# Optimization experiments

Measured on AMD Instinct MI355X. Metric: run time of the kernel, lower is better.

Reference implementation:

```python
import jax, jax.numpy as jnp
import numpy as np

C = 768; NUM_HEADS = 12; HID = 3072
HP = 14; WP = 14; TF = 8; BATCH = 4
EPS = 1e-5


def layer_norm(x, g, b):
    mu = jnp.mean(x, axis=-1, keepdims=True)
    var = jnp.mean((x - mu) ** 2, axis=-1, keepdims=True)
    return (x - mu) / jnp.sqrt(var + EPS) * g + b


def mha(x, qkv_w, qkv_b, proj_w, proj_b):
    # Manual multi-head softmax attention, faithful to Attention.forward.
    B, N, Cd = x.shape
    D = Cd // NUM_HEADS
    qkv = (x @ qkv_w.T + qkv_b).reshape(B, N, 3, NUM_HEADS, D).transpose(2, 0, 3, 1, 4)
    q, k, v = qkv[0], qkv[1], qkv[2]  # [B, H, N, D]
    attn = jax.nn.softmax(jnp.einsum('bhnd,bhmd->bhnm', q, k) * (D ** -0.5), axis=-1)
    out = jnp.einsum('bhnm,bhmd->bhnd', attn, v).transpose(0, 2, 1, 3).reshape(B, N, Cd)
    return out @ proj_w.T + proj_b


def setup_inputs() -> dict:
    key = jax.random.key(0)
    ks = jax.random.split(key, 16)
    p = lambda i, s: jax.random.normal(ks[i], s, jnp.float32) * 0.02
    N = 1 + HP * WP * TF  # cls token + spatial*temporal tokens
    return {
        'x': jax.random.normal(ks[0], (BATCH, N, C), jnp.float32),
        'ln_t_g': jnp.ones((C,), jnp.float32), 'ln_t_b': jnp.zeros((C,), jnp.float32),
        't_qkv_w': p(1, (3 * C, C)), 't_qkv_b': p(2, (3 * C,)),
        't_proj_w': p(3, (C, C)), 't_proj_b': p(4, (C,)),
        't_fc_w': p(5, (C, C)), 't_fc_b': p(6, (C,)),
        'ln1_g': jnp.ones((C,), jnp.float32), 'ln1_b': jnp.zeros((C,), jnp.float32),
        's_qkv_w': p(7, (3 * C, C)), 's_qkv_b': p(8, (3 * C,)),
        's_proj_w': p(9, (C, C)), 's_proj_b': p(10, (C,)),
        'ln2_g': jnp.ones((C,), jnp.float32), 'ln2_b': jnp.zeros((C,), jnp.float32),
        'fc1_w': p(11, (HID, C)), 'fc1_b': p(12, (HID,)),
        'fc2_w': p(13, (C, HID)), 'fc2_b': p(14, (C,)),
        'B': BATCH, 'T': TF, 'W': WP,
    }


def reference(x, ln_t_g, ln_t_b, t_qkv_w, t_qkv_b, t_proj_w, t_proj_b, t_fc_w, t_fc_b,
              ln1_g, ln1_b, s_qkv_w, s_qkv_b, s_proj_w, s_proj_b,
              ln2_g, ln2_b, fc1_w, fc1_b, fc2_w, fc2_b, B, T, W):
    # Block.forward, attention_type='divided_space_time', extra_tokens=0, is_cls=True.
    Bv, Ntot, Cd = x.shape
    H = ((Ntot - 1) // T) // W
    # --- temporal attention: 'b (h w t) m -> (b h w) t m' ---
    xt = x[:, 1:, :].reshape(B, H, W, T, Cd).reshape(B * H * W, T, Cd)
    res_t = mha(layer_norm(xt, ln_t_g, ln_t_b), t_qkv_w, t_qkv_b, t_proj_w, t_proj_b)
    res_t = res_t.reshape(B, H * W * T, Cd) @ t_fc_w.T + t_fc_b
    xt = x[:, 1:, :] + res_t  # [B, H*W*T, C]
    # --- spatial attention: 'b (h w t) m -> (b t) (h w) m' with cls token per frame ---
    init_cls = x[:, :1, :]  # [B, 1, C]
    cls_tok = jnp.repeat(init_cls, T, axis=1).reshape(B * T, 1, Cd)
    xs = xt.reshape(B, H, W, T, Cd).transpose(0, 3, 1, 2, 4).reshape(B * T, H * W, Cd)
    xs = jnp.concatenate([cls_tok, xs], axis=1)  # [(B*T), 1+H*W, C]
    res_s = mha(layer_norm(xs, ln1_g, ln1_b), s_qkv_w, s_qkv_b, s_proj_w, s_proj_b)
    cls_out = jnp.mean(res_s[:, 0, :].reshape(B, T, Cd), axis=1, keepdims=True)  # mean over frames
    res_s = res_s[:, 1:, :].reshape(B, T, H, W, Cd).transpose(0, 2, 3, 1, 4).reshape(B, H * W * T, Cd)
    x = jnp.concatenate([init_cls, xt], axis=1) + jnp.concatenate([cls_out, res_s], axis=1)
    # --- MLP (exact GELU, as nn.GELU default) ---
    h = layer_norm(x, ln2_g, ln2_b)
    h = jax.nn.gelu(h @ fc1_w.T + fc1_b, approximate=False)
    return x + (h @ fc2_w.T + fc2_b)
```

## Files before the change

kernel.cpp:

```cpp
#include <hip/hip_runtime.h>
#include <hip/hip_bf16.h>

typedef __bf16 bf16x8 __attribute__((ext_vector_type(8)));
typedef float f32x4 __attribute__((ext_vector_type(4)));
typedef __hip_bfloat16 bf16;

#define NTOK 1569

__device__ __forceinline__ void gl_lds16(const void* g, void* l) {
  __builtin_amdgcn_global_load_lds(
      (const __attribute__((address_space(1))) void*)g,
      (__attribute__((address_space(3))) void*)l, 16, 0, 0);
}

__device__ __forceinline__ unsigned short bf16bits(float v) {
  union { __hip_bfloat16 h; unsigned short u; } cv;
  cv.h = __float2bfloat16(v);
  return cv.u;
}

__global__ void cvt_bf16_k(const float4* __restrict__ src, uint2* __restrict__ dst, int n4) {
  int i = blockIdx.x * 256 + threadIdx.x;
  if (i < n4) {
    float4 v = src[i];
    union { unsigned short h[4]; uint2 u; } pk;
    pk.h[0] = bf16bits(v.x); pk.h[1] = bf16bits(v.y);
    pk.h[2] = bf16bits(v.z); pk.h[3] = bf16bits(v.w);
    dst[i] = pk.u;
  }
}

__global__ void cvt_t_k(const float* __restrict__ src, bf16* __restrict__ dst) {
  int idx = blockIdx.x * 256 + threadIdx.x;
  int r = idx / 768, c = idx % 768;
  dst[(size_t)c * 768 + r] = __float2bfloat16(src[idx]);
}

__global__ __launch_bounds__(256) void bcomb_k(const float* __restrict__ Wf,
                                               const float* __restrict__ bp,
                                               const float* __restrict__ bfv,
                                               float* __restrict__ out) {
  int j = blockIdx.x * 4 + (threadIdx.x >> 6);
  int l = threadIdx.x & 63;
  if (j >= 768) return;
  float s = 0.f;
#pragma unroll
  for (int u = 0; u < 12; ++u) s += Wf[(size_t)j * 768 + l + 64 * u] * bp[l + 64 * u];
#pragma unroll
  for (int o = 1; o < 64; o <<= 1) s += __shfl_xor(s, o);
  if (l == 0) out[j] = s + bfv[j];
}

__global__ __launch_bounds__(256) void ln_k(
    const float* __restrict__ xsrc, const float* __restrict__ xt,
    const float* __restrict__ gam, const float* __restrict__ bet,
    bf16* __restrict__ y, int M, int mode) {
  int r = blockIdx.x * 4 + (threadIdx.x >> 6);
  int l = threadIdx.x & 63;
  if (r >= M) return;
  const float* src;
  if (mode == 0) {
    src = xsrc + (size_t)(r + r / 1568 + 1) * 768;
  } else {
    int g = r / 197, j = r % 197;
    int b = g >> 3, t = g & 7;
    if (j == 0) src = xsrc + (size_t)b * NTOK * 768;
    else        src = xt + (size_t)(b * 1568 + (j - 1) * 8 + t) * 768;
  }
  const float4* s4 = (const float4*)src;
  const float4* g4 = (const float4*)gam;
  const float4* b4 = (const float4*)bet;
  float4 v[3]; float s = 0.f, s2 = 0.f;
#pragma unroll
  for (int u = 0; u < 3; ++u) {
    float4 t4 = s4[l + 64 * u];
    v[u] = t4;
    s += t4.x + t4.y + t4.z + t4.w;
    s2 += t4.x * t4.x + t4.y * t4.y + t4.z * t4.z + t4.w * t4.w;
  }
#pragma unroll
  for (int o = 1; o < 64; o <<= 1) { s += __shfl_xor(s, o); s2 += __shfl_xor(s2, o); }
  float mu = s * (1.f / 768.f);
  float rstd = rsqrtf(s2 * (1.f / 768.f) - mu * mu + 1e-5f);
  uint2* yr = (uint2*)(y + (size_t)r * 768);
#pragma unroll
  for (int u = 0; u < 3; ++u) {
    int j = l + 64 * u;
    float4 gg = g4[j], bb = b4[j];
    union { unsigned short h[4]; uint2 u2; } pk;
    pk.h[0] = bf16bits((v[u].x - mu) * rstd * gg.x + bb.x);
    pk.h[1] = bf16bits((v[u].y - mu) * rstd * gg.y + bb.y);
    pk.h[2] = bf16bits((v[u].z - mu) * rstd * gg.z + bb.z);
    pk.h[3] = bf16bits((v[u].w - mu) * rstd * gg.w + bb.w);
    yr[j] = pk.u2;
  }
}

__global__ __launch_bounds__(256) void combine_ln_k(
    const float* __restrict__ x, const float* __restrict__ xt,
    const float* __restrict__ rs, const float* __restrict__ gam,
    const float* __restrict__ bet, float* __restrict__ xn,
    bf16* __restrict__ y) {
  int r = blockIdx.x * 4 + (threadIdx.x >> 6);
  int l = threadIdx.x & 63;
  if (r >= 4 * NTOK) return;
  int b = r / NTOK, n = r % NTOK;
  float4 v[3]; float s = 0.f, s2 = 0.f;
  if (n == 0) {
#pragma unroll
    for (int u = 0; u < 3; ++u) {
      int j = l + 64 * u;
      float4 a = {0.f, 0.f, 0.f, 0.f};
#pragma unroll
      for (int t = 0; t < 8; ++t) {
        float4 rv = ((const float4*)(rs + (size_t)((b * 8 + t) * 197) * 768))[j];
        a.x += rv.x; a.y += rv.y; a.z += rv.z; a.w += rv.w;
      }
      float4 xv = ((const float4*)(x + (size_t)r * 768))[j];
      v[u].x = xv.x + a.x * 0.125f; v[u].y = xv.y + a.y * 0.125f;
      v[u].z = xv.z + a.z * 0.125f; v[u].w = xv.w + a.w * 0.125f;
    }
  } else {
    int hw = (n - 1) >> 3, t = (n - 1) & 7;
    const float4* xt4 = (const float4*)(xt + (size_t)(b * 1568 + n - 1) * 768);
    const float4* rs4 = (const float4*)(rs + (size_t)((b * 8 + t) * 197 + 1 + hw) * 768);
#pragma unroll
    for (int u = 0; u < 3; ++u) {
      int j = l + 64 * u;
      float4 a = xt4[j], c = rs4[j];
      v[u].x = a.x + c.x; v[u].y = a.y + c.y; v[u].z = a.z + c.z; v[u].w = a.w + c.w;
    }
  }
  float4* xn4 = (float4*)(xn + (size_t)r * 768);
#pragma unroll
  for (int u = 0; u < 3; ++u) {
    xn4[l + 64 * u] = v[u];
    s += v[u].x + v[u].y + v[u].z + v[u].w;
    s2 += v[u].x * v[u].x + v[u].y * v[u].y + v[u].z * v[u].z + v[u].w * v[u].w;
  }
#pragma unroll
  for (int o = 1; o < 64; o <<= 1) { s += __shfl_xor(s, o); s2 += __shfl_xor(s2, o); }
  float mu = s * (1.f / 768.f);
  float rstd = rsqrtf(s2 * (1.f / 768.f) - mu * mu + 1e-5f);
  const float4* g4 = (const float4*)gam;
  const float4* b4 = (const float4*)bet;
  uint2* yr = (uint2*)(y + (size_t)r * 768);
#pragma unroll
  for (int u = 0; u < 3; ++u) {
    int j = l + 64 * u;
    float4 gg = g4[j], bb = b4[j];
    union { unsigned short h[4]; uint2 u2; } pk;
    pk.h[0] = bf16bits((v[u].x - mu) * rstd * gg.x + bb.x);
    pk.h[1] = bf16bits((v[u].y - mu) * rstd * gg.y + bb.y);
    pk.h[2] = bf16bits((v[u].z - mu) * rstd * gg.z + bb.z);
    pk.h[3] = bf16bits((v[u].w - mu) * rstd * gg.w + bb.w);
    yr[j] = pk.u2;
  }
}

template <int OUTBF16, int RES, int GELU>
__global__ __launch_bounds__(256, 3) void gemm_k(
    const bf16* __restrict__ X, const bf16* __restrict__ W,
    const float* __restrict__ bias, const float* __restrict__ resid,
    void* __restrict__ outp, int M, int N, int K) {
  constexpr int BUFB = 256 * 64;
  __shared__ __align__(16) char LDS[3 * BUFB];
  const int tid = threadIdx.x;
  const int w = tid >> 6, l = tid & 63;
  const int wr = w >> 1, wc = w & 1;
  const int lr = l & 15, lg = l >> 4;

  const int nwg = gridDim.x;
  const int orig = blockIdx.x;
  const int qd = nwg >> 3, rm = nwg & 7;
  const int xcd = orig & 7, lot = orig >> 3;
  const int swz = (xcd < rm ? xcd * (qd + 1) : rm * (qd + 1) + (xcd - rm) * qd) + lot;
  const int ntx = N >> 7;
  const int m0 = (swz / ntx) << 7, n0 = (swz % ntx) << 7;

  const char* pA[2]; const char* pB[2]; int dd[2];
#pragma unroll
  for (int i = 0; i < 2; ++i) {
    int d = (i * 256 + tid) * 16;
    int s = d ^ (((d >> 7) & 3) << 4);
    int r = s >> 6, cb = s & 63;
    int ga = m0 + r; if (ga >= M) ga = M - 1;
    pA[i] = (const char*)X + (size_t)ga * K * 2 + cb;
    pB[i] = (const char*)W + (size_t)(n0 + r) * K * 2 + cb;
    dd[i] = d;
  }

  auto stage = [&](int t, char* buf) {
    size_t ko = (size_t)t * 64;
    gl_lds16(pA[0] + ko, buf + dd[0]);
    gl_lds16(pA[1] + ko, buf + dd[1]);
    gl_lds16(pB[0] + ko, buf + 8192 + dd[0]);
    gl_lds16(pB[1] + ko, buf + 8192 + dd[1]);
  };

  f32x4 acc[4][4] = {};
  auto comp = [&](const char* Ab) {
    const char* Bb = Ab + 8192;
    bf16x8 af[4], bg[4];
#pragma unroll
    for (int mf = 0; mf < 4; ++mf) {
      int d = (wr * 64 + mf * 16 + lr) * 64 + lg * 16;
      af[mf] = *(const bf16x8*)(Ab + (d ^ (((d >> 7) & 3) << 4)));
    }
#pragma unroll
    for (int nf = 0; nf < 4; ++nf) {
      int d = (wc * 64 + nf * 16 + lr) * 64 + lg * 16;
      bg[nf] = *(const bf16x8*)(Bb + (d ^ (((d >> 7) & 3) << 4)));
    }
    __builtin_amdgcn_s_setprio(1);
#pragma unroll
    for (int mf = 0; mf < 4; ++mf)
#pragma unroll
      for (int nf = 0; nf < 4; ++nf)
        acc[mf][nf] = __builtin_amdgcn_mfma_f32_16x16x32_bf16(af[mf], bg[nf], acc[mf][nf], 0, 0, 0);
    __builtin_amdgcn_s_setprio(0);
  };

  const int nt = K >> 5;
  stage(0, LDS);
  stage(1, LDS + BUFB);
  asm volatile("s_waitcnt vmcnt(4)\n\ts_barrier" ::: "memory");
  int t = 0;
#define GSTEP(BC, BS)                                                                      \
  {                                                                                        \
    if (t + 2 < nt) stage(t + 2, LDS + (BS) * BUFB);                                       \
    comp(LDS + (BC) * BUFB);                                                               \
    if (t + 2 < nt)                                                                        \
      asm volatile("s_waitcnt vmcnt(4)\n\ts_barrier" ::: "memory");                        \
    else if (t + 1 < nt)                                                                   \
      asm volatile("s_waitcnt vmcnt(0)\n\ts_barrier" ::: "memory");                        \
    ++t;                                                                                   \
  }
  while (t < nt) { GSTEP(0, 2) GSTEP(1, 0) GSTEP(2, 1) }
#undef GSTEP

#pragma unroll
  for (int mf = 0; mf < 4; ++mf) {
    int rowb = m0 + wr * 64 + mf * 16 + lg * 4;
#pragma unroll
    for (int nf = 0; nf < 4; ++nf) {
      int col = n0 + wc * 64 + nf * 16 + lr;
      float bv = bias ? bias[col] : 0.f;
#pragma unroll
      for (int q = 0; q < 4; ++q) {
        int row = rowb + q;
        if (row < M) {
          float v = acc[mf][nf][q] + bv;
          if (GELU) v = 0.5f * v * (1.f + erff(v * 0.70710678118654752f));
          if (RES == 1) v += resid[(size_t)(row + row / 1568 + 1) * 768 + col];
          if (RES == 2) v += resid[(size_t)row * N + col];
          if (OUTBF16) ((bf16*)outp)[(size_t)row * N + col] = __float2bfloat16(v);
          else         ((float*)outp)[(size_t)row * N + col] = v;
        }
      }
    }
  }
}

__global__ __launch_bounds__(256) void attn_t_k(const bf16* __restrict__ qkv,
                                                bf16* __restrict__ outp) {
  __shared__ float sh[4][3 * 8 * 68];
  const int wv = threadIdx.x >> 6, l = threadIdx.x & 63;
  const int g = blockIdx.x * 4 + wv;
  const int sq = g / 12, hd = g % 12;
  float* qs = sh[wv];
  float* ks = qs + 544;
  float* vs = qs + 1088;
  const bf16* base = qkv + (size_t)sq * 8 * 2304 + hd * 64;
  {
    int row = l >> 3, c8 = (l & 7) * 8;
    const bf16* rp = base + (size_t)row * 2304 + c8;
    bf16x8 qv = *(const bf16x8*)rp;
    bf16x8 kv = *(const bf16x8*)(rp + 768);
    bf16x8 vv = *(const bf16x8*)(rp + 1536);
    float* qd = qs + row * 68 + c8;
    float* kd = ks + row * 68 + c8;
    float* vd = vs + row * 68 + c8;
    float4 a, b;
    a.x = (float)qv[0]; a.y = (float)qv[1]; a.z = (float)qv[2]; a.w = (float)qv[3];
    b.x = (float)qv[4]; b.y = (float)qv[5]; b.z = (float)qv[6]; b.w = (float)qv[7];
    *(float4*)qd = a; *(float4*)(qd + 4) = b;
    a.x = (float)kv[0]; a.y = (float)kv[1]; a.z = (float)kv[2]; a.w = (float)kv[3];
    b.x = (float)kv[4]; b.y = (float)kv[5]; b.z = (float)kv[6]; b.w = (float)kv[7];
    *(float4*)kd = a; *(float4*)(kd + 4) = b;
    a.x = (float)vv[0]; a.y = (float)vv[1]; a.z = (float)vv[2]; a.w = (float)vv[3];
    b.x = (float)vv[4]; b.y = (float)vv[5]; b.z = (float)vv[6]; b.w = (float)vv[7];
    *(float4*)vd = a; *(float4*)(vd + 4) = b;
  }
  __builtin_amdgcn_wave_barrier();
  const int i = l >> 3, j = l & 7;
  float s = 0.f;
#pragma unroll
  for (int d = 0; d < 64; ++d) s += qs[i * 68 + d] * ks[j * 68 + d];
  s *= 0.125f;
  float m = s;
  m = fmaxf(m, __shfl_xor(m, 1));
  m = fmaxf(m, __shfl_xor(m, 2));
  m = fmaxf(m, __shfl_xor(m, 4));
  float p = __expf(s - m);
  float sum = p;
  sum += __shfl_xor(sum, 1);
  sum += __shfl_xor(sum, 2);
  sum += __shfl_xor(sum, 4);
  p /= sum;
  float pr[8];
#pragma unroll
  for (int jj = 0; jj < 8; ++jj) pr[jj] = __shfl(p, i * 8 + jj);
  bf16* op = outp + (size_t)(sq * 8) * 768 + hd * 64;
#pragma unroll
  for (int u = 0; u < 8; ++u) {
    int c = j + 8 * u;
    float o = 0.f;
#pragma unroll
    for (int jj = 0; jj < 8; ++jj) o += pr[jj] * vs[jj * 68 + c];
    op[(size_t)i * 768 + c] = __float2bfloat16(o);
  }
}

__global__ __launch_bounds__(256) void build_vt_k(const bf16* __restrict__ qkv,
                                                  bf16* __restrict__ vt) {
  const int sq = blockIdx.x / 12, hd = blockIdx.x % 12;
  const bf16* vsrc = qkv + (size_t)sq * 197 * 2304 + 1536 + hd * 64;
  bf16* dst = vt + (size_t)blockIdx.x * 64 * 224;
  for (int idx = threadIdx.x; idx < 197 * 64; idx += 256) {
    int j = idx >> 6, d = idx & 63;
    dst[d * 224 + j] = vsrc[(size_t)j * 2304 + d];
  }
}

__global__ __launch_bounds__(256) void attn_s_k(
    const bf16* __restrict__ qkv, const bf16* __restrict__ vt,
    bf16* __restrict__ outp) {
  __shared__ __align__(16) bf16 P[4][16 * 232];
  const int wv = threadIdx.x >> 6, l = threadIdx.x & 63;
  const int sq = blockIdx.x / 12, hd = blockIdx.x % 12;
  const int lr = l & 15, lg = l >> 4;
  bf16* Pw = P[wv];
#pragma unroll
  for (int idx = 0; idx < 4; ++idx) {
    int e = idx * 64 + l;
    Pw[(e >> 4) * 232 + 208 + (e & 15)] = __float2bfloat16(0.f);
  }
  const bf16* qbase = qkv + (size_t)sq * 197 * 2304 + hd * 64;
  const bf16* kbase = qbase + 768;
  const bf16* vbase = vt + (size_t)blockIdx.x * 64 * 224;
  for (int qt = wv; qt < 13; qt += 4) {
    int q0 = qt * 16;
    int qrow = q0 + lr; if (qrow > 196) qrow = 196;
    bf16x8 qa0 = *(const bf16x8*)(qbase + (size_t)qrow * 2304 + lg * 8);
    bf16x8 qa1 = *(const bf16x8*)(qbase + (size_t)qrow * 2304 + 32 + lg * 8);
    f32x4 sacc[13];
#pragma unroll
    for (int jt = 0; jt < 13; ++jt) {
      const bf16* kp = kbase + (size_t)(jt * 16 + lr) * 2304;
      bf16x8 kb0 = *(const bf16x8*)(kp + lg * 8);
      bf16x8 kb1 = *(const bf16x8*)(kp + 32 + lg * 8);
      f32x4 z = {};
      z = __builtin_amdgcn_mfma_f32_16x16x32_bf16(qa0, kb0, z, 0, 0, 0);
      z = __builtin_amdgcn_mfma_f32_16x16x32_bf16(qa1, kb1, z, 0, 0, 0);
      sacc[jt] = z;
    }
#pragma unroll
    for (int jt = 0; jt < 13; ++jt) {
      bool valid = (jt * 16 + lr) < 197;
#pragma unroll
      for (int q = 0; q < 4; ++q)
        sacc[jt][q] = valid ? sacc[jt][q] * 0.125f : -3e38f;
    }
    float inv[4];
#pragma unroll
    for (int q = 0; q < 4; ++q) {
      float m = -3e38f;
#pragma unroll
      for (int jt = 0; jt < 13; ++jt) m = fmaxf(m, sacc[jt][q]);
      m = fmaxf(m, __shfl_xor(m, 1));
      m = fmaxf(m, __shfl_xor(m, 2));
      m = fmaxf(m, __shfl_xor(m, 4));
      m = fmaxf(m, __shfl_xor(m, 8));
      float ssum = 0.f;
#pragma unroll
      for (int jt = 0; jt < 13; ++jt) {
        float p = __expf(sacc[jt][q] - m);
        sacc[jt][q] = p;
        ssum += p;
      }
      ssum += __shfl_xor(ssum, 1);
      ssum += __shfl_xor(ssum, 2);
      ssum += __shfl_xor(ssum, 4);
      ssum += __shfl_xor(ssum, 8);
      inv[q] = 1.f / ssum;
    }
#pragma unroll
    for (int jt = 0; jt < 13; ++jt)
#pragma unroll
      for (int q = 0; q < 4; ++q)
        Pw[(lg * 4 + q) * 232 + jt * 16 + lr] = __float2bfloat16(sacc[jt][q]);
    __builtin_amdgcn_wave_barrier();
    f32x4 oacc[4] = {};
#pragma unroll
    for (int j7 = 0; j7 < 7; ++j7) {
      bf16x8 pa = *(const bf16x8*)(Pw + lr * 232 + j7 * 32 + lg * 8);
#pragma unroll
      for (int n = 0; n < 4; ++n) {
        bf16x8 vb = *(const bf16x8*)(vbase + (size_t)(n * 16 + lr) * 224 + j7 * 32 + lg * 8);
        oacc[n] = __builtin_amdgcn_mfma_f32_16x16x32_bf16(pa, vb, oacc[n], 0, 0, 0);
      }
    }
    __builtin_amdgcn_wave_barrier();
#pragma unroll
    for (int n = 0; n < 4; ++n)
#pragma unroll
      for (int q = 0; q < 4; ++q) {
        int orow = q0 + lg * 4 + q;
        if (orow < 197)
          outp[(size_t)(sq * 197 + orow) * 768 + hd * 64 + n * 16 + lr] =
              __float2bfloat16(oacc[n][q] * inv[q]);
      }
  }
}

extern "C" void kernel_launch(void* const* d_in, const int* in_sizes, int n_in,
                              void* d_out, int out_size, void* d_ws, size_t ws_size,
                              hipStream_t stream) {
  (void)in_sizes; (void)n_in; (void)out_size; (void)ws_size;
  const float* x        = (const float*)d_in[0];
  const float* ln_t_g   = (const float*)d_in[1];
  const float* ln_t_b   = (const float*)d_in[2];
  const float* t_qkv_w  = (const float*)d_in[3];
  const float* t_qkv_b  = (const float*)d_in[4];
  const float* t_proj_w = (const float*)d_in[5];
  const float* t_proj_b = (const float*)d_in[6];
  const float* t_fc_w   = (const float*)d_in[7];
  const float* t_fc_b   = (const float*)d_in[8];
  const float* ln1_g    = (const float*)d_in[9];
  const float* ln1_b    = (const float*)d_in[10];
  const float* s_qkv_w  = (const float*)d_in[11];
  const float* s_qkv_b  = (const float*)d_in[12];
  const float* s_proj_w = (const float*)d_in[13];
  const float* s_proj_b = (const float*)d_in[14];
  const float* ln2_g    = (const float*)d_in[15];
  const float* ln2_b    = (const float*)d_in[16];
  const float* fc1_w    = (const float*)d_in[17];
  const float* fc1_b    = (const float*)d_in[18];
  const float* fc2_w    = (const float*)d_in[19];
  const float* fc2_b    = (const float*)d_in[20];

  char* ws = (char*)d_ws;
  size_t o = 0;
  auto alloc = [&](size_t bytes) { size_t r = o; o += (bytes + 255) & ~(size_t)255; return r; };
  bf16* wqkvt  = (bf16*)(ws + alloc((size_t)2304 * 768 * 2));
  bf16* wqkvs  = (bf16*)(ws + alloc((size_t)2304 * 768 * 2));
  bf16* wprojs = (bf16*)(ws + alloc((size_t)768 * 768 * 2));
  bf16* wfct   = (bf16*)(ws + alloc((size_t)768 * 768 * 2));
  bf16* wpT    = (bf16*)(ws + alloc((size_t)768 * 768 * 2));
  bf16* wcomb  = (bf16*)(ws + alloc((size_t)768 * 768 * 2));
  float* bcomb = (float*)(ws + alloc((size_t)768 * 4));
  bf16* wfc1   = (bf16*)(ws + alloc((size_t)3072 * 768 * 2));
  bf16* wfc2   = (bf16*)(ws + alloc((size_t)768 * 3072 * 2));
  bf16* ybuf   = (bf16*)(ws + alloc((size_t)6400 * 768 * 2));
  char* big    = ws + alloc((size_t)6400 * 3072 * 2);
  bf16* qkvb   = (bf16*)big;
  bf16* h1     = (bf16*)big;
  bf16* abuf   = (bf16*)(ws + alloc((size_t)6400 * 768 * 2));
  char* slotS  = ws + alloc((size_t)6304 * 768 * 4);
  bf16* vtb    = (bf16*)slotS;
  float* rsb   = (float*)slotS;
  float* xtb   = (float*)(ws + alloc((size_t)6272 * 768 * 4));
  float* xnb   = (float*)(ws + alloc((size_t)6276 * 768 * 4));

  cvt_bf16_k<<<1728, 256, 0, stream>>>((const float4*)t_qkv_w, (uint2*)wqkvt, 442368);
  cvt_bf16_k<<<1728, 256, 0, stream>>>((const float4*)s_qkv_w, (uint2*)wqkvs, 442368);
  cvt_bf16_k<<<576, 256, 0, stream>>>((const float4*)s_proj_w, (uint2*)wprojs, 147456);
  cvt_bf16_k<<<576, 256, 0, stream>>>((const float4*)t_fc_w, (uint2*)wfct, 147456);
  cvt_t_k<<<2304, 256, 0, stream>>>(t_proj_w, wpT);
  cvt_bf16_k<<<2304, 256, 0, stream>>>((const float4*)fc1_w, (uint2*)wfc1, 589824);
  cvt_bf16_k<<<2304, 256, 0, stream>>>((const float4*)fc2_w, (uint2*)wfc2, 589824);
  bcomb_k<<<192, 256, 0, stream>>>(t_fc_w, t_proj_b, t_fc_b, bcomb);
  gemm_k<1, 0, 0><<<36, 256, 0, stream>>>(wfct, wpT, nullptr, nullptr, wcomb, 768, 768, 768);

  ln_k<<<1568, 256, 0, stream>>>(x, nullptr, ln_t_g, ln_t_b, ybuf, 6272, 0);
  gemm_k<1, 0, 0><<<882, 256, 0, stream>>>(ybuf, wqkvt, t_qkv_b, nullptr, qkvb, 6272, 2304, 768);
  attn_t_k<<<2352, 256, 0, stream>>>(qkvb, abuf);
  gemm_k<0, 1, 0><<<294, 256, 0, stream>>>(abuf, wcomb, bcomb, x, xtb, 6272, 768, 768);

  ln_k<<<1576, 256, 0, stream>>>(x, xtb, ln1_g, ln1_b, ybuf, 6304, 1);
  gemm_k<1, 0, 0><<<900, 256, 0, stream>>>(ybuf, wqkvs, s_qkv_b, nullptr, qkvb, 6304, 2304, 768);
  build_vt_k<<<384, 256, 0, stream>>>(qkvb, vtb);
  attn_s_k<<<384, 256, 0, stream>>>(qkvb, vtb, abuf);
  gemm_k<0, 0, 0><<<300, 256, 0, stream>>>(abuf, wprojs, s_proj_b, nullptr, rsb, 6304, 768, 768);

  combine_ln_k<<<1569, 256, 0, stream>>>(x, xtb, rsb, ln2_g, ln2_b, xnb, ybuf);

  gemm_k<1, 0, 1><<<1200, 256, 0, stream>>>(ybuf, wfc1, fc1_b, nullptr, h1, 6276, 3072, 768);
  gemm_k<0, 2, 0><<<300, 256, 0, stream>>>(h1, wfc2, fc2_b, xnb, (float*)d_out, 6276, 768, 3072);
}
```

Before: 565.0 us.

## Add 64x64-tile GEMM for N=768 projections and fuse weight conversions

Adds a new 64x64 output-tile GEMM kernel with a 4-deep LDS ring fed by direct global-to-LDS loads, swizzled addressing, XCD-aware block remapping and occupancy hint 4. It replaces the 128x128-tile GEMM for the four N=768 GEMMs, which previously launched only about 300 workgroups and underfilled the GPU. Six separate fp32-to-bf16 weight conversion launches are also merged into one segmented kernel to cut launch overhead. Smaller tiles mean less operand reuse per workgroup and more global traffic, especially for the K=3072 fc2 GEMM.

```diff
diff --git a/kernel.cpp b/kernel.cpp
--- a/kernel.cpp
+++ b/kernel.cpp
@@ -19,15 +19,23 @@
   return cv.u;
 }
 
-__global__ void cvt_bf16_k(const float4* __restrict__ src, uint2* __restrict__ dst, int n4) {
+struct CvtSeg { const float4* src; uint2* dst; int end; };
+__global__ void cvt_all_k(CvtSeg s0, CvtSeg s1, CvtSeg s2, CvtSeg s3, CvtSeg s4, CvtSeg s5) {
   int i = blockIdx.x * 256 + threadIdx.x;
-  if (i < n4) {
-    float4 v = src[i];
-    union { unsigned short h[4]; uint2 u; } pk;
-    pk.h[0] = bf16bits(v.x); pk.h[1] = bf16bits(v.y);
-    pk.h[2] = bf16bits(v.z); pk.h[3] = bf16bits(v.w);
-    dst[i] = pk.u;
-  }
+  CvtSeg s; int base = 0;
+  if (i < s0.end) { s = s0; }
+  else if (i < s1.end) { s = s1; base = s0.end; }
+  else if (i < s2.end) { s = s2; base = s1.end; }
+  else if (i < s3.end) { s = s3; base = s2.end; }
+  else if (i < s4.end) { s = s4; base = s3.end; }
+  else if (i < s5.end) { s = s5; base = s4.end; }
+  else return;
+  int j = i - base;
+  float4 v = s.src[j];
+  union { unsigned short h[4]; uint2 u; } pk;
+  pk.h[0] = bf16bits(v.x); pk.h[1] = bf16bits(v.y);
+  pk.h[2] = bf16bits(v.z); pk.h[3] = bf16bits(v.w);
+  s.dst[j] = pk.u;
 }
 
 __global__ void cvt_t_k(const float* __restrict__ src, bf16* __restrict__ dst) {
@@ -257,6 +265,106 @@
           if (OUTBF16) ((bf16*)outp)[(size_t)row * N + col] = __float2bfloat16(v);
           else         ((float*)outp)[(size_t)row * N + col] = v;
         }
+      }
+    }
+  }
+}
+
+template <int OUTBF16, int RES, int GELU>
+__global__ __launch_bounds__(256, 4) void gemm64(
+    const bf16* __restrict__ X, const bf16* __restrict__ W,
+    const float* __restrict__ bias, const float* __restrict__ resid,
+    void* __restrict__ outp, int M, int N, int K) {
+  constexpr int BUFB = 128 * 64;
+  __shared__ __align__(16) char LDS[4 * BUFB];
+  const int tid = threadIdx.x;
+  const int wc = tid >> 6, l = tid & 63;
+  const int lr = l & 15, lg = l >> 4;
+
+  const int nwg = gridDim.x;
+  const int orig = blockIdx.x;
+  const int qd = nwg >> 3, rm = nwg & 7;
+  const int xcd = orig & 7, lot = orig >> 3;
+  const int swz = (xcd < rm ? xcd * (qd + 1) : rm * (qd + 1) + (xcd - rm) * qd) + lot;
+  const int ntx = N >> 6;
+  const int m0 = (swz / ntx) << 6, n0 = (swz % ntx) << 6;
+
+  const char* pS[2]; int dd[2];
+#pragma unroll
+  for (int i = 0; i < 2; ++i) {
+    int d = (i * 256 + tid) * 16;
+    int s = d ^ (((d >> 7) & 3) << 4);
+    int r = s >> 6, cb = s & 63;
+    if (i == 0) {
+      int ga = m0 + r; if (ga >= M) ga = M - 1;
+      pS[0] = (const char*)X + (size_t)ga * K * 2 + cb;
+    } else {
+      pS[1] = (const char*)W + (size_t)(n0 + (r - 64)) * K * 2 + cb;
+    }
+    dd[i] = d;
+  }
+
+  auto stage = [&](int t, char* buf) {
+    size_t ko = (size_t)t * 64;
+    gl_lds16(pS[0] + ko, buf + dd[0]);
+    gl_lds16(pS[1] + ko, buf + dd[1]);
+  };
+
+  f32x4 acc[4] = {};
+  auto comp = [&](const char* buf) {
+    bf16x8 af[4], bg;
+#pragma unroll
+    for (int mf = 0; mf < 4; ++mf) {
+      int d = (mf * 16 + lr) * 64 + lg * 16;
+      af[mf] = *(const bf16x8*)(buf + (d ^ (((d >> 7) & 3) << 4)));
+    }
+    {
+      int d = (64 + wc * 16 + lr) * 64 + lg * 16;
+      bg = *(const bf16x8*)(buf + (d ^ (((d >> 7) & 3) << 4)));
+    }
+    __builtin_amdgcn_s_setprio(1);
+#pragma unroll
+    for (int mf = 0; mf < 4; ++mf)
+      acc[mf] = __builtin_amdgcn_mfma_f32_16x16x32_bf16(af[mf], bg, acc[mf], 0, 0, 0);
+    __builtin_amdgcn_s_setprio(0);
+  };
+
+  const int nt = K >> 5;
+  stage(0, LDS);
+  stage(1, LDS + BUFB);
+  stage(2, LDS + 2 * BUFB);
+  asm volatile("s_waitcnt vmcnt(4)\n\ts_barrier" ::: "memory");
+  int t = 0;
+#define GSTEP(BC, BS)                                                                      \
+  {                                                                                        \
+    if (t + 3 < nt) stage(t + 3, LDS + (BS) * BUFB);                                       \
+    comp(LDS + (BC) * BUFB);                                                               \
+    if (t + 3 < nt)                                                                        \
+      asm volatile("s_waitcnt vmcnt(4)\n\ts_barrier" ::: "memory");                        \
+    else if (t + 2 < nt)                                                                   \
+      asm volatile("s_waitcnt vmcnt(2)\n\ts_barrier" ::: "memory");                        \
+    else if (t + 1 < nt)                                                                   \
+      asm volatile("s_waitcnt vmcnt(0)\n\ts_barrier" ::: "memory");                        \
+    ++t;                                                                                   \
+  }
+  while (t < nt) { GSTEP(0, 3) GSTEP(1, 0) GSTEP(2, 1) GSTEP(3, 2) }
+#undef GSTEP
+
+#pragma unroll
+  for (int mf = 0; mf < 4; ++mf) {
+    int rowb = m0 + mf * 16 + lg * 4;
+    int col = n0 + wc * 16 + lr;
+    float bv = bias ? bias[col] : 0.f;
+#pragma unroll
+    for (int q = 0; q < 4; ++q) {
+      int row = rowb + q;
+      if (row < M) {
+        float v = acc[mf][q] + bv;
+        if (GELU) v = 0.5f * v * (1.f + erff(v * 0.70710678118654752f));
+        if (RES == 1) v += resid[(size_t)(row + row / 1568 + 1) * 768 + col];
+        if (RES == 2) v += resid[(size_t)row * N + col];
+        if (OUTBF16) ((bf16*)outp)[(size_t)row * N + col] = __float2bfloat16(v);
+        else         ((float*)outp)[(size_t)row * N + col] = v;
       }
     }
   }
@@ -473,29 +581,32 @@
   float* xtb   = (float*)(ws + alloc((size_t)6272 * 768 * 4));
   float* xnb   = (float*)(ws + alloc((size_t)6276 * 768 * 4));
 
-  cvt_bf16_k<<<1728, 256, 0, stream>>>((const float4*)t_qkv_w, (uint2*)wqkvt, 442368);
-  cvt_bf16_k<<<1728, 256, 0, stream>>>((const float4*)s_qkv_w, (uint2*)wqkvs, 442368);
-  cvt_bf16_k<<<576, 256, 0, stream>>>((const float4*)s_proj_w, (uint2*)wprojs, 147456);
-  cvt_bf16_k<<<576, 256, 0, stream>>>((const float4*)t_fc_w, (uint2*)wfct, 147456);
+  {
+    CvtSeg s0{(const float4*)t_qkv_w, (uint2*)wqkvt, 442368};
+    CvtSeg s1{(const float4*)s_qkv_w, (uint2*)wqkvs, 442368 + 442368};
+    CvtSeg s2{(const float4*)s_proj_w, (uint2*)wprojs, 884736 + 147456};
+    CvtSeg s3{(const float4*)t_fc_w, (uint2*)wfct, 1032192 + 147456};
+    CvtSeg s4{(const float4*)fc1_w, (uint2*)wfc1, 1179648 + 589824};
+    CvtSeg s5{(const float4*)fc2_w, (uint2*)wfc2, 1769472 + 589824};
+    cvt_all_k<<<(2359296 + 255) / 256, 256, 0, stream>>>(s0, s1, s2, s3, s4, s5);
+  }
   cvt_t_k<<<2304, 256, 0, stream>>>(t_proj_w, wpT);
-  cvt_bf16_k<<<2304, 256, 0, stream>>>((const float4*)fc1_w, (uint2*)wfc1, 589824);
-  cvt_bf16_k<<<2304, 256, 0, stream>>>((const float4*)fc2_w, (uint2*)wfc2, 589824);
   bcomb_k<<<192, 256, 0, stream>>>(t_fc_w, t_proj_b, t_fc_b, bcomb);
-  gemm_k<1, 0, 0><<<36, 256, 0, stream>>>(wfct, wpT, nullptr, nullptr, wcomb, 768, 768, 768);
+  gemm64<1, 0, 0><<<144, 256, 0, stream>>>(wfct, wpT, nullptr, nullptr, wcomb, 768, 768, 768);
 
   ln_k<<<1568, 256, 0, stream>>>(x, nullptr, ln_t_g, ln_t_b, ybuf, 6272, 0);
   gemm_k<1, 0, 0><<<882, 256, 0, stream>>>(ybuf, wqkvt, t_qkv_b, nullptr, qkvb, 6272, 2304, 768);
   attn_t_k<<<2352, 256, 0, stream>>>(qkvb, abuf);
-  gemm_k<0, 1, 0><<<294, 256, 0, stream>>>(abuf, wcomb, bcomb, x, xtb, 6272, 768, 768);
+  gemm64<0, 1, 0><<<1176, 256, 0, stream>>>(abuf, wcomb, bcomb, x, xtb, 6272, 768, 768);
 
   ln_k<<<1576, 256, 0, stream>>>(x, xtb, ln1_g, ln1_b, ybuf, 6304, 1);
   gemm_k<1, 0, 0><<<900, 256, 0, stream>>>(ybuf, wqkvs, s_qkv_b, nullptr, qkvb, 6304, 2304, 768);
   build_vt_k<<<384, 256, 0, stream>>>(qkvb, vtb);
   attn_s_k<<<384, 256, 0, stream>>>(qkvb, vtb, abuf);
-  gemm_k<0, 0, 0><<<300, 256, 0, stream>>>(abuf, wprojs, s_proj_b, nullptr, rsb, 6304, 768, 768);
+  gemm64<0, 0, 0><<<1188, 256, 0, stream>>>(abuf, wprojs, s_proj_b, nullptr, rsb, 6304, 768, 768);
 
   combine_ln_k<<<1569, 256, 0, stream>>>(x, xtb, rsb, ln2_g, ln2_b, xnb, ybuf);
 
   gemm_k<1, 0, 1><<<1200, 256, 0, stream>>>(ybuf, wfc1, fc1_b, nullptr, h1, 6276, 3072, 768);
-  gemm_k<0, 2, 0><<<300, 256, 0, stream>>>(h1, wfc2, fc2_b, xnb, (float*)d_out, 6276, 768, 3072);
-}
+  gemm64<0, 2, 0><<<1188, 256, 0, stream>>>(h1, wfc2, fc2_b, xnb, (float*)d_out, 6276, 768, 3072);
+}
```

Result: faster. 540.6 us (-4.3%).
